# Kernel tuning notes

Measured on AMD Instinct MI355X. Metric: run time of the kernel, lower is better.

## Reference

```python
import jax, jax.numpy as jnp
import numpy as np

NUM_HEADS = 8

def setup_inputs() -> dict:
    key = jax.random.key(0)
    k1, k2, k3, k4 = jax.random.split(key, 4)
    B, C, H, W = 8, 512, 32, 32
    x = jax.random.normal(k1, (B, C, H, W), dtype=jnp.float32)
    # Conv2d 1x1 weights flattened to [out, in]
    w_qkv = jax.random.normal(k2, (3 * C, C), dtype=jnp.float32) * (C ** -0.5)
    w_proj = jax.random.normal(k3, (C, C), dtype=jnp.float32) * (C ** -0.5)
    b_proj = jax.random.normal(k4, (C,), dtype=jnp.float32) * 0.02
    return {"x": x, "w_qkv": w_qkv, "w_proj": w_proj, "b_proj": b_proj}

def reference(x, w_qkv, w_proj, b_proj):
    B, C, H, W = x.shape
    nh = NUM_HEADS
    hd = C // nh
    N = H * W
    scale = hd ** -0.5
    xf = x.reshape(B, C, N)
    # 1x1 conv == per-pixel GEMM; reshape 3C channels as (nh, 3*hd) per torch reshape
    qkv = jnp.einsum('oc,bcn->bon', w_qkv, xf).reshape(B, nh, 3 * hd, N)
    q, k, v = jnp.split(qkv, 3, axis=2)  # each [B, nh, hd, N]
    # attn[b,h,nk,nq] = sum_d k[b,h,d,nk] * q[b,h,d,nq]
    attn = jnp.einsum('bhdn,bhdm->bhnm', k, q) * scale
    attn = jax.nn.softmax(attn, axis=-2)  # softmax over key axis (dim=-2), as in source
    out = jnp.einsum('bhdn,bhnm->bhdm', v, attn).reshape(B, C, H, W)
    out = jnp.einsum('oc,bchw->bohw', w_proj, out) + b_proj[None, :, None, None]
    return out
```

## Files before the change

kernel.cpp:

```cpp
#include <hip/hip_runtime.h>
#include <math.h>


typedef unsigned int u32;
typedef float  f32x4 __attribute__((ext_vector_type(4)));
typedef short  s16x8 __attribute__((ext_vector_type(8)));
typedef unsigned short u16x4 __attribute__((ext_vector_type(4)));
typedef unsigned int   u32x2 __attribute__((ext_vector_type(2)));
typedef unsigned int   u32x4 __attribute__((ext_vector_type(4)));

#define MFMA16(a, b, c) __builtin_amdgcn_mfma_f32_16x16x32_bf16(a, b, c, 0, 0, 0)

__device__ __forceinline__ ushort f2bf(float f) {
    u32 b = __float_as_uint(f);
    return (ushort)((b + 0x7FFFu + ((b >> 16) & 1u)) >> 16);
}
__device__ __forceinline__ float bf2f(ushort v) {
    return __uint_as_float(((u32)v) << 16);
}
__device__ __forceinline__ u32 cvtpk(float a, float b) {
    u32 r;
    asm("v_cvt_pk_bf16_f32 %0, %1, %2" : "=v"(r) : "v"(a), "v"(b));
    return r;
}

__global__ __launch_bounds__(256) void prep(
    const float* __restrict__ x, const float* __restrict__ wq,
    const float* __restrict__ wp, ushort* __restrict__ xh,
    ushort* __restrict__ wq_s, ushort* __restrict__ wp_s) {
    __shared__ __align__(16) ushort Th[64 * 72];
    const int t = threadIdx.x;

    {
        const int id = (blockIdx.z * 8 + blockIdx.y) * 16 + blockIdx.x;
        size_t base = ((size_t)id * 256 + t) * 4;
        const float* src; ushort* dst; size_t off;
        if (base < 786432) { src = wq; dst = wq_s; off = base; }
        else               { src = wp; dst = wp_s; off = base - 786432; }
        f32x4 v = *(const f32x4*)(src + off);
        u16x4 s;
#pragma unroll
        for (int e = 0; e < 4; e++) s[e] = f2bf(v[e]);
        *(u16x4*)(dst + off) = s;
    }

    const int n0 = blockIdx.x * 64, c0 = blockIdx.y * 64, b = blockIdx.z;
    const int c = t >> 2, nseg = (t & 3) * 4;
    const float* src = x + ((size_t)b * 512 + c0 + c) * 1024 + n0;
#pragma unroll
    for (int i = 0; i < 4; i++) {
        f32x4 v = *(const f32x4*)(src + nseg + i * 16);
#pragma unroll
        for (int e = 0; e < 4; e++) {
            int nl = nseg + i * 16 + e;
            Th[nl * 72 + c] = f2bf(v[e]);
        }
    }
    __syncthreads();
#pragma unroll
    for (int i = 0; i < 2; i++) {
        int nl = i * 32 + (t >> 3);
        int u = t & 7;
        s16x8 vh = *(const s16x8*)(Th + nl * 72 + u * 8);
        size_t go = ((size_t)b * 1024 + n0 + nl) * 512 + c0 + u * 8;
        *(s16x8*)(xh + go) = vh;
    }
}

__device__ __forceinline__ void gemm_core1(
    const ushort* __restrict__ A_g, int arow0,
    const ushort* __restrict__ B_g, size_t brow0,
    ushort* smem, f32x4 (&acc)[4][4]) {
    const int t = threadIdx.x;
    ushort* As = smem;
    ushort* Bs = smem + 5120;
    const int ro = t >> 1, cs = (t & 1) << 4;
    const size_t ga = (size_t)(arow0 + ro) * 512 + cs;
    const size_t gb = (brow0 + ro) * 512 + cs;
    const int l15 = t & 15, quad = (t >> 4) & 3, wv = t >> 6;
    const int lra = (((wv >> 1) * 64) + l15) * 40 + quad * 8;
    const int lrb = (((wv & 1) * 64) + l15) * 40 + quad * 8;
    const int lw = ro * 40 + cs;

    s16x8 va0 = *(const s16x8*)(A_g + ga), va1 = *(const s16x8*)(A_g + ga + 8);
    s16x8 vb0 = *(const s16x8*)(B_g + gb), vb1 = *(const s16x8*)(B_g + gb + 8);

    for (int k0 = 0; k0 < 512; k0 += 32) {
        __syncthreads();
        *(s16x8*)(As + lw) = va0; *(s16x8*)(As + lw + 8) = va1;
        *(s16x8*)(Bs + lw) = vb0; *(s16x8*)(Bs + lw + 8) = vb1;
        const int kn = (k0 + 32) & 511;
        va0 = *(const s16x8*)(A_g + ga + kn); va1 = *(const s16x8*)(A_g + ga + kn + 8);
        vb0 = *(const s16x8*)(B_g + gb + kn); vb1 = *(const s16x8*)(B_g + gb + kn + 8);
        __syncthreads();
        s16x8 a[4], bb[4];
#pragma unroll
        for (int Mt = 0; Mt < 4; Mt++)
            a[Mt] = *(const s16x8*)(As + lra + Mt * 640);
#pragma unroll
        for (int Nt = 0; Nt < 4; Nt++)
            bb[Nt] = *(const s16x8*)(Bs + lrb + Nt * 640);
#pragma unroll
        for (int Mt = 0; Mt < 4; Mt++)
#pragma unroll
            for (int Nt = 0; Nt < 4; Nt++)
                acc[Mt][Nt] = MFMA16(a[Mt], bb[Nt], acc[Mt][Nt]);
    }
    __syncthreads();
}

__global__ __launch_bounds__(256) void gemm_qkv(
    const ushort* __restrict__ wq_s, const ushort* __restrict__ xt_h,
    ushort* __restrict__ qT, ushort* __restrict__ kT, ushort* __restrict__ vT) {
    __shared__ __align__(16) ushort smem[10240];
    f32x4 acc[4][4];
#pragma unroll
    for (int i = 0; i < 4; i++)
#pragma unroll
        for (int j = 0; j < 4; j++) acc[i][j] = (f32x4)0.0f;

    const int n0 = blockIdx.x * 128, o0 = blockIdx.y * 128, bz = blockIdx.z;
    gemm_core1(wq_s, o0, xt_h, (size_t)bz * 1024 + n0, smem, acc);

    const int t = threadIdx.x;
    const int l15 = t & 15, quad = (t >> 4) & 3, wv = t >> 6, lane = t & 63;
    const int g = blockIdx.y * 2 + (wv >> 1);
    const int role = g % 3, head = g / 3;
    const int nh = (wv & 1) * 64;
    const size_t hb = (size_t)bz * 8 + head;
    const float scale = (role == 0) ? 0.18033688011112042f : 1.0f;

    if (role < 2) {
        ushort* dst = (role == 0) ? qT : kT;
        ushort* T = smem + wv * 2304;
        const size_t rowbase = hb * 1024 + n0 + nh;
#pragma unroll
        for (int sp = 0; sp < 2; sp++) {
#pragma unroll
            for (int Mti = 0; Mti < 2; Mti++)
#pragma unroll
                for (int Nt = 0; Nt < 4; Nt++) {
                    f32x4 v = acc[sp * 2 + Mti][Nt];
                    u32x2 pk;
                    pk.x = cvtpk(v[0] * scale, v[1] * scale);
                    pk.y = cvtpk(v[2] * scale, v[3] * scale);
                    *(u32x2*)(T + (Nt * 16 + l15) * 36 + Mti * 16 + quad * 4) = pk;
                }
            asm volatile("s_waitcnt lgkmcnt(0)" ::: "memory");
#pragma unroll
            for (int i = 0; i < 8; i++) {
                int nl = i * 8 + (lane >> 3);
                u16x4 vv = *(const u16x4*)(T + nl * 36 + (lane & 7) * 4);
                *(u16x4*)(dst + (rowbase + nl) * 64 + sp * 32 + (lane & 7) * 4) = vv;
            }
            asm volatile("s_waitcnt lgkmcnt(0)" ::: "memory");
        }
    } else {
        const size_t vb2 = hb * 64 * 1024 + (size_t)(n0 + nh);
#pragma unroll
        for (int Mt = 0; Mt < 4; Mt++)
#pragma unroll
            for (int Nt = 0; Nt < 4; Nt++)
#pragma unroll
                for (int r = 0; r < 4; r++)
                    vT[vb2 + (size_t)(Mt * 16 + quad * 4 + r) * 1024 + Nt * 16 + l15] =
                        f2bf(acc[Mt][Nt][r]);
    }
}

__global__ __launch_bounds__(256) void gemm_proj(
    const ushort* __restrict__ wp_s, const ushort* __restrict__ ht,
    const float* __restrict__ bias, float* __restrict__ out) {
    __shared__ __align__(16) ushort smem[10240];
    f32x4 acc[4][4];
#pragma unroll
    for (int i = 0; i < 4; i++)
#pragma unroll
        for (int j = 0; j < 4; j++) acc[i][j] = (f32x4)0.0f;

    const int n0 = blockIdx.x * 128, o0 = blockIdx.y * 128, bz = blockIdx.z;
    gemm_core1(wp_s, o0, ht, (size_t)bz * 1024 + n0, smem, acc);

    const int t = threadIdx.x;
    const int l15 = t & 15, quad = (t >> 4) & 3, wv = t >> 6;
#pragma unroll
    for (int Mt = 0; Mt < 4; Mt++)
#pragma unroll
        for (int Nt = 0; Nt < 4; Nt++) {
            int ob = o0 + (wv >> 1) * 64 + Mt * 16 + quad * 4;
            int nn = n0 + (wv & 1) * 64 + Nt * 16 + l15;
#pragma unroll
            for (int r = 0; r < 4; r++)
                out[((size_t)bz * 512 + ob + r) * 1024 + nn] = acc[Mt][Nt][r] + bias[ob + r];
        }
}

__global__ __launch_bounds__(256, 2) void attn_mfma(
    const ushort* __restrict__ qT, const ushort* __restrict__ kT,
    const ushort* __restrict__ vT, ushort* __restrict__ ht) {
    __shared__ __align__(16) ushort Ps[4 * 4352];
    __shared__ float Ls[4][64];
    const int t = threadIdx.x;
    const int id = blockIdx.x + (blockIdx.y << 4);
    const int swz = (id & 7) * 128 + (id >> 3);
    const int qt = swz & 15, bh = swz >> 4;
    const int b = bh >> 3, h = bh & 7;
    const int m0 = qt * 64;
    const int l15 = t & 15, quad = (t >> 4) & 3, wv = t >> 6;

    s16x8 qf[4][2];
#pragma unroll
    for (int Nt = 0; Nt < 4; Nt++) {
        const size_t qb = ((size_t)bh * 1024 + m0 + Nt * 16 + l15) * 64 + quad * 8;
        qf[Nt][0] = *(const s16x8*)(qT + qb);
        qf[Nt][1] = *(const s16x8*)(qT + qb + 32);
    }

    f32x4 O[4][4];
#pragma unroll
    for (int i = 0; i < 4; i++)
#pragma unroll
        for (int j = 0; j < 4; j++) O[i][j] = (f32x4)0.0f;
    float lrun[4] = {0.f, 0.f, 0.f, 0.f};

    const ushort* kb = kT + (size_t)bh * 65536;
    const ushort* vb = vT + (size_t)bh * 65536;
    ushort* Pw = Ps + wv * 4352;

    s16x8 kf[2][4], vf[2][4];
    {
        const int kt = wv * 4;
        const size_t kbase = (size_t)kt * 4096 + l15 * 64 + quad * 8;
        const size_t vbase = (size_t)l15 * 1024 + kt * 64 + quad * 8;
#pragma unroll
        for (int ks = 0; ks < 2; ks++)
#pragma unroll
            for (int Mt = 0; Mt < 4; Mt++) {
                kf[ks][Mt] = *(const s16x8*)(kb + kbase + Mt * 1024 + ks * 32);
                vf[ks][Mt] = *(const s16x8*)(vb + vbase + Mt * 16384 + ks * 32);
            }
    }

#pragma unroll 1
    for (int i = 0; i < 4; i++) {
        const int ktn = wv * 4 + i + 1;

#pragma unroll
        for (int g2 = 0; g2 < 2; g2++) {
            f32x4 S[4][2];
#pragma unroll
            for (int a = 0; a < 4; a++) { S[a][0] = (f32x4)0.0f; S[a][1] = (f32x4)0.0f; }
            __builtin_amdgcn_s_setprio(1);
#pragma unroll
            for (int ks = 0; ks < 2; ks++)
#pragma unroll
                for (int Mt = 0; Mt < 4; Mt++)
#pragma unroll
                    for (int n2 = 0; n2 < 2; n2++)
                        S[Mt][n2] = MFMA16(kf[ks][Mt], qf[g2 * 2 + n2][ks], S[Mt][n2]);
            __builtin_amdgcn_s_setprio(0);

            if (g2 == 1 && i < 3) {
                const size_t kbase = (size_t)ktn * 4096 + l15 * 64 + quad * 8;
#pragma unroll
                for (int ks = 0; ks < 2; ks++)
#pragma unroll
                    for (int Mt = 0; Mt < 4; Mt++)
                        kf[ks][Mt] = *(const s16x8*)(kb + kbase + Mt * 1024 + ks * 32);
            }

#pragma unroll
            for (int n2 = 0; n2 < 2; n2++) {
#pragma unroll
                for (int Mt = 0; Mt < 4; Mt++)
#pragma unroll
                    for (int r = 0; r < 4; r++)
                        S[Mt][n2][r] = __builtin_amdgcn_exp2f(S[Mt][n2][r]);
                float s0 = (S[0][n2][0] + S[0][n2][1]) + (S[0][n2][2] + S[0][n2][3]);
                float s1 = (S[1][n2][0] + S[1][n2][1]) + (S[1][n2][2] + S[1][n2][3]);
                float s2 = (S[2][n2][0] + S[2][n2][1]) + (S[2][n2][2] + S[2][n2][3]);
                float s3 = (S[3][n2][0] + S[3][n2][1]) + (S[3][n2][2] + S[3][n2][3]);
                lrun[g2 * 2 + n2] += (s0 + s1) + (s2 + s3);
            }
#pragma unroll
            for (int Mt = 0; Mt < 4; Mt++)
#pragma unroll
                for (int n2 = 0; n2 < 2; n2++) {
                    u32x2 pb;
                    pb.x = cvtpk(S[Mt][n2][0], S[Mt][n2][1]);
                    pb.y = cvtpk(S[Mt][n2][2], S[Mt][n2][3]);
                    *(u32x2*)(Pw + ((g2 * 2 + n2) * 16 + l15) * 68 + Mt * 16 + quad * 4) = pb;
                }
        }

#pragma unroll
        for (int ks = 0; ks < 2; ks++) {
            s16x8 pf[4];
#pragma unroll
            for (int Nt = 0; Nt < 4; Nt++)
                pf[Nt] = *(const s16x8*)(Pw + (Nt * 16 + l15) * 68 + ks * 32 + quad * 8);
            __builtin_amdgcn_s_setprio(1);
#pragma unroll
            for (int Mt = 0; Mt < 4; Mt++)
#pragma unroll
                for (int Nt = 0; Nt < 4; Nt++)
                    O[Mt][Nt] = MFMA16(vf[ks][Mt], pf[Nt], O[Mt][Nt]);
            __builtin_amdgcn_s_setprio(0);
        }

        if (i < 3) {
            const size_t vbase = (size_t)l15 * 1024 + ktn * 64 + quad * 8;
#pragma unroll
            for (int ks = 0; ks < 2; ks++)
#pragma unroll
                for (int Mt = 0; Mt < 4; Mt++)
                    vf[ks][Mt] = *(const s16x8*)(vb + vbase + Mt * 16384 + ks * 32);
        }
    }

#pragma unroll
    for (int Mt = 0; Mt < 4; Mt++)
#pragma unroll
        for (int Nt = 0; Nt < 4; Nt++) {
            u32x2 pk;
            pk.x = cvtpk(O[Mt][Nt][0], O[Mt][Nt][1]);
            pk.y = cvtpk(O[Mt][Nt][2], O[Mt][Nt][3]);
            *(u32x2*)(Pw + (Nt * 16 + l15) * 68 + Mt * 16 + quad * 4) = pk;
        }
#pragma unroll
    for (int Nt = 0; Nt < 4; Nt++) {
        float ts = lrun[Nt];
        ts += __shfl_xor(ts, 16);
        ts += __shfl_xor(ts, 32);
        if (quad == 0) Ls[wv][Nt * 16 + l15] = ts;
    }
    __syncthreads();

    const int q = t >> 2, ds = (t & 3) * 16;
    const float l = Ls[0][q] + Ls[1][q] + Ls[2][q] + Ls[3][q];
    const float linv = 1.f / l;
    float acc[16];
#pragma unroll
    for (int e = 0; e < 16; e++) acc[e] = 0.f;
#pragma unroll
    for (int w = 0; w < 4; w++) {
        s16x8 a0 = *(const s16x8*)(Ps + w * 4352 + q * 68 + ds);
        s16x8 a1 = *(const s16x8*)(Ps + w * 4352 + q * 68 + ds + 8);
#pragma unroll
        for (int e = 0; e < 8; e++) {
            acc[e] += bf2f((ushort)a0[e]);
            acc[8 + e] += bf2f((ushort)a1[e]);
        }
    }
    u32x4 r0, r1;
#pragma unroll
    for (int e = 0; e < 4; e++) {
        r0[e] = cvtpk(acc[2 * e] * linv, acc[2 * e + 1] * linv);
        r1[e] = cvtpk(acc[8 + 2 * e] * linv, acc[9 + 2 * e] * linv);
    }
    const size_t go = ((size_t)b * 1024 + m0 + q) * 512 + h * 64 + ds;
    *(u32x4*)(ht + go) = r0;
    *(u32x4*)(ht + go + 8) = r1;
}

extern "C" void kernel_launch(void* const* d_in, const int* in_sizes, int n_in,
                              void* d_out, int out_size, void* d_ws, size_t ws_size,
                              hipStream_t stream) {
    (void)in_sizes; (void)n_in; (void)out_size; (void)ws_size;
    const float* x      = (const float*)d_in[0];
    const float* w_qkv  = (const float*)d_in[1];
    const float* w_proj = (const float*)d_in[2];
    const float* b_proj = (const float*)d_in[3];
    float* out = (float*)d_out;

    char* ws = (char*)d_ws;
    ushort* xt_h = (ushort*)(ws);
    ushort* wq_s = (ushort*)(ws + 8388608);
    ushort* wp_s = (ushort*)(ws + 9961472);
    ushort* qT   = (ushort*)(ws + 10485760);
    ushort* kT   = (ushort*)(ws + 18874368);
    ushort* vT   = (ushort*)(ws + 27262976);
    ushort* ht   = xt_h;

    prep<<<dim3(16, 8, 8), 256, 0, stream>>>(x, w_qkv, w_proj, xt_h,
                                             wq_s, wp_s);
    gemm_qkv<<<dim3(8, 12, 8), 256, 0, stream>>>(wq_s, xt_h, qT, kT, vT);
    attn_mfma<<<dim3(16, 64), 256, 0, stream>>>(qT, kT, vT, ht);
    gemm_proj<<<dim3(8, 4, 8), 256, 0, stream>>>(wp_s, xt_h, b_proj, out);
}
```

Before: 147.7 us.

## Software-pipeline attention score and PV MFMAs; retile projection GEMM to 64x128

The attention inner loop is restructured so the score MFMAs for one half of the key tile overlap with the PV MFMAs of the previous tile's second half. The exp/convert work of one group is interleaved with MFMAs of another, and the V fragment loads are split so each half is refetched just after it is consumed. The projection GEMM gets its own smaller 64x128 tile with register-prefetched global loads, doubling the block count to improve occupancy and wave count. The cost is more complex ordering of shared-memory P writes and reads across iterations, which risks hazards and higher register pressure.

```diff
diff --git a/kernel.cpp b/kernel.cpp
--- a/kernel.cpp
+++ b/kernel.cpp
@@ -171,24 +171,58 @@
 __global__ __launch_bounds__(256) void gemm_proj(
     const ushort* __restrict__ wp_s, const ushort* __restrict__ ht,
     const float* __restrict__ bias, float* __restrict__ out) {
-    __shared__ __align__(16) ushort smem[10240];
-    f32x4 acc[4][4];
+    __shared__ __align__(16) ushort smem[7680];
+    ushort* As = smem;
+    ushort* Bs = smem + 2560;
+    f32x4 acc[4][2];
 #pragma unroll
     for (int i = 0; i < 4; i++)
 #pragma unroll
-        for (int j = 0; j < 4; j++) acc[i][j] = (f32x4)0.0f;
-
-    const int n0 = blockIdx.x * 128, o0 = blockIdx.y * 128, bz = blockIdx.z;
-    gemm_core1(wp_s, o0, ht, (size_t)bz * 1024 + n0, smem, acc);
-
+        for (int j = 0; j < 2; j++) acc[i][j] = (f32x4)0.0f;
+
+    const int n0 = blockIdx.x * 128, o0 = blockIdx.y * 64, bz = blockIdx.z;
     const int t = threadIdx.x;
+    const int roa = t >> 2, csa = (t & 3) * 8;
+    const size_t ga = (size_t)(o0 + roa) * 512 + csa;
+    const int rob = t >> 1, csb = (t & 1) << 4;
+    const size_t gb = ((size_t)bz * 1024 + n0 + rob) * 512 + csb;
     const int l15 = t & 15, quad = (t >> 4) & 3, wv = t >> 6;
+    const int lra = l15 * 40 + quad * 8;
+    const int lrb = (wv * 32 + l15) * 40 + quad * 8;
+    const int lwa = roa * 40 + csa;
+    const int lwb = rob * 40 + csb;
+
+    s16x8 va  = *(const s16x8*)(wp_s + ga);
+    s16x8 vb0 = *(const s16x8*)(ht + gb), vb1 = *(const s16x8*)(ht + gb + 8);
+
+    for (int k0 = 0; k0 < 512; k0 += 32) {
+        __syncthreads();
+        *(s16x8*)(As + lwa) = va;
+        *(s16x8*)(Bs + lwb) = vb0; *(s16x8*)(Bs + lwb + 8) = vb1;
+        const int kn = (k0 + 32) & 511;
+        va  = *(const s16x8*)(wp_s + ga + kn);
+        vb0 = *(const s16x8*)(ht + gb + kn); vb1 = *(const s16x8*)(ht + gb + kn + 8);
+        __syncthreads();
+        s16x8 a[4], bb[2];
+#pragma unroll
+        for (int Mt = 0; Mt < 4; Mt++)
+            a[Mt] = *(const s16x8*)(As + lra + Mt * 640);
+#pragma unroll
+        for (int Nt = 0; Nt < 2; Nt++)
+            bb[Nt] = *(const s16x8*)(Bs + lrb + Nt * 640);
+#pragma unroll
+        for (int Mt = 0; Mt < 4; Mt++)
+#pragma unroll
+            for (int Nt = 0; Nt < 2; Nt++)
+                acc[Mt][Nt] = MFMA16(a[Mt], bb[Nt], acc[Mt][Nt]);
+    }
+
 #pragma unroll
     for (int Mt = 0; Mt < 4; Mt++)
 #pragma unroll
-        for (int Nt = 0; Nt < 4; Nt++) {
-            int ob = o0 + (wv >> 1) * 64 + Mt * 16 + quad * 4;
-            int nn = n0 + (wv & 1) * 64 + Nt * 16 + l15;
+        for (int Nt = 0; Nt < 2; Nt++) {
+            int ob = o0 + Mt * 16 + quad * 4;
+            int nn = n0 + wv * 32 + Nt * 16 + l15;
 #pragma unroll
             for (int r = 0; r < 4; r++)
                 out[((size_t)bz * 512 + ob + r) * 1024 + nn] = acc[Mt][Nt][r] + bias[ob + r];
@@ -245,77 +279,140 @@
     for (int i = 0; i < 4; i++) {
         const int ktn = wv * 4 + i + 1;
 
-#pragma unroll
-        for (int g2 = 0; g2 < 2; g2++) {
-            f32x4 S[4][2];
-#pragma unroll
-            for (int a = 0; a < 4; a++) { S[a][0] = (f32x4)0.0f; S[a][1] = (f32x4)0.0f; }
+        f32x4 SA[2][4];
+#pragma unroll
+        for (int m = 0; m < 2; m++)
+#pragma unroll
+            for (int qa = 0; qa < 4; qa++) SA[m][qa] = (f32x4)0.0f;
+        __builtin_amdgcn_s_setprio(1);
+#pragma unroll
+        for (int ks = 0; ks < 2; ks++)
+#pragma unroll
+            for (int m = 0; m < 2; m++)
+#pragma unroll
+                for (int qa = 0; qa < 4; qa++)
+                    SA[m][qa] = MFMA16(kf[ks][m], qf[qa][ks], SA[m][qa]);
+
+        if (i > 0) {
+            s16x8 pf1[4];
+#pragma unroll
+            for (int Nt = 0; Nt < 4; Nt++)
+                pf1[Nt] = *(const s16x8*)(Pw + (Nt * 16 + l15) * 68 + 32 + quad * 8);
+#pragma unroll
+            for (int Mt = 0; Mt < 4; Mt++)
+#pragma unroll
+                for (int Nt = 0; Nt < 4; Nt++)
+                    O[Mt][Nt] = MFMA16(vf[1][Mt], pf1[Nt], O[Mt][Nt]);
+        }
+        __builtin_amdgcn_s_setprio(0);
+
+        if (i > 0) {
+            const size_t vbase = (size_t)l15 * 1024 + (wv * 4 + i) * 64 + quad * 8;
+#pragma unroll
+            for (int Mt = 0; Mt < 4; Mt++)
+                vf[1][Mt] = *(const s16x8*)(vb + vbase + Mt * 16384 + 32);
+        }
+
+#pragma unroll
+        for (int qa = 0; qa < 4; qa++) {
+#pragma unroll
+            for (int m = 0; m < 2; m++)
+#pragma unroll
+                for (int r = 0; r < 4; r++)
+                    SA[m][qa][r] = __builtin_amdgcn_exp2f(SA[m][qa][r]);
+            float s0 = (SA[0][qa][0] + SA[0][qa][1]) + (SA[0][qa][2] + SA[0][qa][3]);
+            float s1 = (SA[1][qa][0] + SA[1][qa][1]) + (SA[1][qa][2] + SA[1][qa][3]);
+            lrun[qa] += s0 + s1;
+        }
+#pragma unroll
+        for (int qa = 0; qa < 4; qa++)
+#pragma unroll
+            for (int m = 0; m < 2; m++) {
+                u32x2 pb;
+                pb.x = cvtpk(SA[m][qa][0], SA[m][qa][1]);
+                pb.y = cvtpk(SA[m][qa][2], SA[m][qa][3]);
+                *(u32x2*)(Pw + (qa * 16 + l15) * 68 + m * 16 + quad * 4) = pb;
+            }
+
+        f32x4 SB[2][4];
+#pragma unroll
+        for (int m = 0; m < 2; m++)
+#pragma unroll
+            for (int qa = 0; qa < 4; qa++) SB[m][qa] = (f32x4)0.0f;
+        __builtin_amdgcn_s_setprio(1);
+#pragma unroll
+        for (int ks = 0; ks < 2; ks++)
+#pragma unroll
+            for (int m = 0; m < 2; m++)
+#pragma unroll
+                for (int qa = 0; qa < 4; qa++)
+                    SB[m][qa] = MFMA16(kf[ks][m + 2], qf[qa][ks], SB[m][qa]);
+        __builtin_amdgcn_s_setprio(0);
+
+        if (i < 3) {
+            const size_t kbase = (size_t)ktn * 4096 + l15 * 64 + quad * 8;
+#pragma unroll
+            for (int ks = 0; ks < 2; ks++)
+#pragma unroll
+                for (int Mt = 0; Mt < 4; Mt++)
+                    kf[ks][Mt] = *(const s16x8*)(kb + kbase + Mt * 1024 + ks * 32);
+        }
+
+        {
+            s16x8 pf0[4];
+#pragma unroll
+            for (int Nt = 0; Nt < 4; Nt++)
+                pf0[Nt] = *(const s16x8*)(Pw + (Nt * 16 + l15) * 68 + quad * 8);
             __builtin_amdgcn_s_setprio(1);
 #pragma unroll
-            for (int ks = 0; ks < 2; ks++)
-#pragma unroll
-                for (int Mt = 0; Mt < 4; Mt++)
-#pragma unroll
-                    for (int n2 = 0; n2 < 2; n2++)
-                        S[Mt][n2] = MFMA16(kf[ks][Mt], qf[g2 * 2 + n2][ks], S[Mt][n2]);
-            __builtin_amdgcn_s_setprio(0);
-
-            if (g2 == 1 && i < 3) {
-                const size_t kbase = (size_t)ktn * 4096 + l15 * 64 + quad * 8;
-#pragma unroll
-                for (int ks = 0; ks < 2; ks++)
-#pragma unroll
-                    for (int Mt = 0; Mt < 4; Mt++)
-                        kf[ks][Mt] = *(const s16x8*)(kb + kbase + Mt * 1024 + ks * 32);
-            }
-
-#pragma unroll
-            for (int n2 = 0; n2 < 2; n2++) {
-#pragma unroll
-                for (int Mt = 0; Mt < 4; Mt++)
-#pragma unroll
-                    for (int r = 0; r < 4; r++)
-                        S[Mt][n2][r] = __builtin_amdgcn_exp2f(S[Mt][n2][r]);
-                float s0 = (S[0][n2][0] + S[0][n2][1]) + (S[0][n2][2] + S[0][n2][3]);
-                float s1 = (S[1][n2][0] + S[1][n2][1]) + (S[1][n2][2] + S[1][n2][3]);
-                float s2 = (S[2][n2][0] + S[2][n2][1]) + (S[2][n2][2] + S[2][n2][3]);
-                float s3 = (S[3][n2][0] + S[3][n2][1]) + (S[3][n2][2] + S[3][n2][3]);
-                lrun[g2 * 2 + n2] += (s0 + s1) + (s2 + s3);
-            }
-#pragma unroll
             for (int Mt = 0; Mt < 4; Mt++)
 #pragma unroll
-                for (int n2 = 0; n2 < 2; n2++) {
-                    u32x2 pb;
-                    pb.x = cvtpk(S[Mt][n2][0], S[Mt][n2][1]);
-                    pb.y = cvtpk(S[Mt][n2][2], S[Mt][n2][3]);
-                    *(u32x2*)(Pw + ((g2 * 2 + n2) * 16 + l15) * 68 + Mt * 16 + quad * 4) = pb;
-                }
-        }
-
-#pragma unroll
-        for (int ks = 0; ks < 2; ks++) {
-            s16x8 pf[4];
-#pragma unroll
-            for (int Nt = 0; Nt < 4; Nt++)
-                pf[Nt] = *(const s16x8*)(Pw + (Nt * 16 + l15) * 68 + ks * 32 + quad * 8);
-            __builtin_amdgcn_s_setprio(1);
-#pragma unroll
-            for (int Mt = 0; Mt < 4; Mt++)
-#pragma unroll
                 for (int Nt = 0; Nt < 4; Nt++)
-                    O[Mt][Nt] = MFMA16(vf[ks][Mt], pf[Nt], O[Mt][Nt]);
+                    O[Mt][Nt] = MFMA16(vf[0][Mt], pf0[Nt], O[Mt][Nt]);
             __builtin_amdgcn_s_setprio(0);
         }
 
         if (i < 3) {
             const size_t vbase = (size_t)l15 * 1024 + ktn * 64 + quad * 8;
 #pragma unroll
-            for (int ks = 0; ks < 2; ks++)
-#pragma unroll
-                for (int Mt = 0; Mt < 4; Mt++)
-                    vf[ks][Mt] = *(const s16x8*)(vb + vbase + Mt * 16384 + ks * 32);
-        }
+            for (int Mt = 0; Mt < 4; Mt++)
+                vf[0][Mt] = *(const s16x8*)(vb + vbase + Mt * 16384);
+        }
+
+#pragma unroll
+        for (int qa = 0; qa < 4; qa++) {
+#pragma unroll
+            for (int m = 0; m < 2; m++)
+#pragma unroll
+                for (int r = 0; r < 4; r++)
+                    SB[m][qa][r] = __builtin_amdgcn_exp2f(SB[m][qa][r]);
+            float s0 = (SB[0][qa][0] + SB[0][qa][1]) + (SB[0][qa][2] + SB[0][qa][3]);
+            float s1 = (SB[1][qa][0] + SB[1][qa][1]) + (SB[1][qa][2] + SB[1][qa][3]);
+            lrun[qa] += s0 + s1;
+        }
+#pragma unroll
+        for (int qa = 0; qa < 4; qa++)
+#pragma unroll
+            for (int m = 0; m < 2; m++) {
+                u32x2 pb;
+                pb.x = cvtpk(SB[m][qa][0], SB[m][qa][1]);
+                pb.y = cvtpk(SB[m][qa][2], SB[m][qa][3]);
+                *(u32x2*)(Pw + (qa * 16 + l15) * 68 + (m + 2) * 16 + quad * 4) = pb;
+            }
+    }
+
+    {
+        s16x8 pf1[4];
+#pragma unroll
+        for (int Nt = 0; Nt < 4; Nt++)
+            pf1[Nt] = *(const s16x8*)(Pw + (Nt * 16 + l15) * 68 + 32 + quad * 8);
+        __builtin_amdgcn_s_setprio(1);
+#pragma unroll
+        for (int Mt = 0; Mt < 4; Mt++)
+#pragma unroll
+            for (int Nt = 0; Nt < 4; Nt++)
+                O[Mt][Nt] = MFMA16(vf[1][Mt], pf1[Nt], O[Mt][Nt]);
+        __builtin_amdgcn_s_setprio(0);
     }
 
 #pragma unroll
@@ -386,5 +483,5 @@
                                              wq_s, wp_s);
     gemm_qkv<<<dim3(8, 12, 8), 256, 0, stream>>>(wq_s, xt_h, qT, kT, vT);
     attn_mfma<<<dim3(16, 64), 256, 0, stream>>>(qT, kT, vT, ht);
-    gemm_proj<<<dim3(8, 4, 8), 256, 0, stream>>>(wp_s, xt_h, b_proj, out);
-}
+    gemm_proj<<<dim3(8, 8, 8), 256, 0, stream>>>(wp_s, xt_h, b_proj, out);
+}
```

Result: slower. 199.8 us (+35.3%).
